# Optimization experiments

Hardware: AMD Instinct MI355X
Metric: run time of the kernel (lower is better)

Reference implementation:

```python
import jax, jax.numpy as jnp
import numpy as np

S_DIM = 8      # state_dim
O_DIM = 4      # obs_dim
HID = (S_DIM * S_DIM + O_DIM * O_DIM) * 10   # 800
BATCH = 128
SEQ = 32
NS = 16        # num_samples
P_DROP = 0.2
DROP_KEY = jax.random.key(42)

def f_dyn(x):
    # synthetic nonlinear dynamics (stand-in for system_model.f, vmapped over batch)
    return 0.9 * x + 0.1 * jnp.sin(x)

def h_obs(x):
    # synthetic nonlinear observation (stand-in for system_model.h)
    return jnp.tanh(x[..., :O_DIM])

def l2_normalize(x, eps=1e-12):
    # matches torch F.normalize(p=2, dim=1): x / max(||x||, eps)
    n = jnp.linalg.norm(x, axis=-1, keepdims=True)
    return x / jnp.maximum(n, eps)

def setup_inputs() -> dict:
    key = jax.random.key(0)
    ks = jax.random.split(key, 8)
    g = 0.02
    return {
        "y_seq": jax.random.normal(ks[0], (BATCH, SEQ, O_DIM), dtype=jnp.float32),
        "W1": jax.random.normal(ks[1], (HID, S_DIM + O_DIM), dtype=jnp.float32) * g,
        "b1": jnp.zeros((HID,), jnp.float32),
        "W_ih": jax.random.normal(ks[2], (3 * HID, HID), dtype=jnp.float32) * g,
        "W_hh": jax.random.normal(ks[3], (3 * HID, HID), dtype=jnp.float32) * g,
        "b_ih": jnp.zeros((3 * HID,), jnp.float32),
        "b_hh": jnp.zeros((3 * HID,), jnp.float32),
        "W_out": jax.random.normal(ks[4], (S_DIM * O_DIM, HID), dtype=jnp.float32) * g,
        "b_out": jnp.zeros((S_DIM * O_DIM,), jnp.float32),
        "num_samples": NS,
    }

def _forward(y_seq, W1, b1, W_ih, W_hh, b_ih, b_hh, W_out, b_out, num_samples):
    B = y_seq.shape[0]
    keep = 1.0 - P_DROP

    def gru_cell(x, h):
        # torch nn.GRU single-step math; x,h: [..., HID]
        gi = x @ W_ih.T + b_ih
        gh = h @ W_hh.T + b_hh
        gi_r, gi_z, gi_n = jnp.split(gi, 3, axis=-1)
        gh_r, gh_z, gh_n = jnp.split(gh, 3, axis=-1)
        r = jax.nn.sigmoid(gi_r + gh_r)
        z = jax.nn.sigmoid(gi_z + gh_z)
        n = jnp.tanh(gi_n + r * gh_n)
        return (1.0 - z) * n + z * h

    def step(carry, inp):
        x_prev, dx_prev, h_ens = carry            # [B,S], [B,S], [NS,B,HID]
        y_t, t = inp
        x_pred = f_dyn(x_prev)                    # [B,S] (same for every sample j)
        y_hat = h_obs(x_pred)                     # [B,O]
        innov = y_t - y_hat                       # [B,O]
        nn_in = jnp.concatenate([l2_normalize(dx_prev), l2_normalize(innov)], axis=-1)
        a = jax.nn.relu(nn_in @ W1.T + b1)        # [B,HID]
        k1, k2 = jax.random.split(jax.random.fold_in(DROP_KEY, t))
        m1 = jax.random.bernoulli(k1, keep, (num_samples, B, HID)).astype(a.dtype)
        a_ens = a[None] * m1 / keep               # MC-dropout per ensemble member
        h_new = gru_cell(a_ens, h_ens)            # [NS,B,HID] (vectorized over samples)
        K_vec = h_new @ W_out.T + b_out           # [NS,B,S*O]
        m2 = jax.random.bernoulli(k2, keep, K_vec.shape).astype(a.dtype)
        K = (K_vec * m2 / keep).reshape(num_samples, B, S_DIM, O_DIM)
        ens = x_pred[None] + jnp.einsum('jbso,bo->jbs', K, innov)  # [NS,B,S]
        x_filt = ens.mean(axis=0)                 # [B,S]
        diff = ens - x_filt[None]                 # [NS,B,S]
        P_filt = jnp.einsum('jbs,jbt->bst', diff, diff) / num_samples
        dx = x_filt - x_pred                      # delta_x_prev = x_filt - f(x_prev)
        return (x_filt, dx, h_new), (x_filt, P_filt)

    x0 = jnp.zeros((B, S_DIM), y_seq.dtype)
    dx0 = jnp.zeros((B, S_DIM), y_seq.dtype)
    h0 = jnp.zeros((num_samples, B, HID), y_seq.dtype)
    ts = jnp.arange(y_seq.shape[1])
    _, (xs, Ps) = jax.lax.scan(step, (x0, dx0, h0), (jnp.swapaxes(y_seq, 0, 1), ts))
    # xs: [T,B,S] -> [B,T,S]; Ps: [T,B,S,S] -> [B,T,S,S]
    return jnp.swapaxes(xs, 0, 1), jnp.swapaxes(Ps, 0, 1)

def reference(y_seq, W1, b1, W_ih, W_hh, b_ih, b_hh, W_out, b_out, num_samples):
    return _forward(y_seq, W1, b1, W_ih, W_hh, b_ih, b_hh, W_out, b_out, num_samples)
```

## Files before the change

kernel.cpp:

```cpp
#include <hip/hip_runtime.h>
#include <stdint.h>

#define NSAMP 16
#define BATCH 128
#define SEQLEN 32
#define SDIM 8
#define ODIM 4
#define HID 800
#define MROWS (NSAMP * BATCH)
#define KEEPP 0.8f

typedef __attribute__((ext_vector_type(8))) short short8v;
typedef __attribute__((ext_vector_type(4))) float float4v;

__host__ __device__ __forceinline__ void tf2x32(uint32_t k0, uint32_t k1,
                                                uint32_t x0, uint32_t x1,
                                                uint32_t& o0, uint32_t& o1) {
  uint32_t ks2 = k0 ^ k1 ^ 0x1BD11BDAu;
  x0 += k0; x1 += k1;
#define TFR(r) { x0 += x1; x1 = (x1 << (r)) | (x1 >> (32 - (r))); x1 ^= x0; }
  TFR(13) TFR(15) TFR(26) TFR(6)
  x0 += k1; x1 += ks2 + 1u;
  TFR(17) TFR(29) TFR(16) TFR(24)
  x0 += ks2; x1 += k0 + 2u;
  TFR(13) TFR(15) TFR(26) TFR(6)
  x0 += k0; x1 += k1 + 3u;
  TFR(17) TFR(29) TFR(16) TFR(24)
  x0 += k1; x1 += ks2 + 4u;
  TFR(13) TFR(15) TFR(26) TFR(6)
  x0 += ks2; x1 += k0 + 5u;
#undef TFR
  o0 = x0; o1 = x1;
}

__device__ __forceinline__ float bits_to_unit(uint32_t bits) {
  return __uint_as_float((bits >> 9) | 0x3F800000u) - 1.0f;
}

__device__ __forceinline__ float tf_uniform_part(uint32_t k0, uint32_t k1, uint32_t idx) {
  uint32_t b1, b2;
  tf2x32(k0, k1, 0u, idx, b1, b2);
  return bits_to_unit(b1 ^ b2);
}

__device__ __forceinline__ ushort f2bf(float f) {
  uint32_t u = __float_as_uint(f);
  uint32_t r = (u + 0x7FFFu + ((u >> 16) & 1u)) >> 16;
  return (ushort)r;
}

__device__ __forceinline__ float bf2f(ushort u) {
  return __uint_as_float((uint32_t)u << 16);
}

__device__ __forceinline__ void bar_sync() {
  __builtin_amdgcn_sched_barrier(0);
  __builtin_amdgcn_s_barrier();
  __builtin_amdgcn_sched_barrier(0);
}

__global__ void convert_w_kernel(const float* __restrict__ W_ih, const float* __restrict__ W_hh,
                                 ushort* __restrict__ Wib, ushort* __restrict__ Whb) {
  int i = (blockIdx.x * 256 + threadIdx.x) * 4;
  if (i >= 2400 * HID) return;
  float4 v1 = *reinterpret_cast<const float4*>(W_ih + i);
  float4 v2 = *reinterpret_cast<const float4*>(W_hh + i);
  ushort4 o1, o2;
  o1.x = f2bf(v1.x); o1.y = f2bf(v1.y); o1.z = f2bf(v1.z); o1.w = f2bf(v1.w);
  o2.x = f2bf(v2.x); o2.y = f2bf(v2.y); o2.z = f2bf(v2.z); o2.w = f2bf(v2.w);
  *reinterpret_cast<ushort4*>(Wib + i) = o1;
  *reinterpret_cast<ushort4*>(Whb + i) = o2;
}

__global__ void transpose_wout_kernel(const float* __restrict__ W_out, float* __restrict__ WoutT) {
  int i = blockIdx.x * 256 + threadIdx.x;
  if (i < 32 * HID) {
    int o = i / HID, k = i - o * HID;
    WoutT[k * 32 + o] = W_out[i];
  }
}

__global__ void a_ens_kernel(const float* __restrict__ a, ushort* __restrict__ aeb,
                             uint32_t k0, uint32_t k1) {
  int base = (blockIdx.x * blockDim.x + threadIdx.x) * 4;
  if (base >= MROWS * HID) return;
  int row = base / HID;
  int b = row % BATCH;
  int col = base - row * HID;
  float4 av = *reinterpret_cast<const float4*>(a + b * HID + col);
  ushort4 ov;
#pragma unroll
  for (int q = 0; q < 4; ++q) {
    float u = tf_uniform_part(k0, k1, (uint32_t)(base + q));
    float f = (&av.x)[q] * ((u < KEEPP) ? 1.25f : 0.0f);
    (&ov.x)[q] = f2bf(f);
  }
  *reinterpret_cast<ushort4*>(aeb + base) = ov;
}

#define LDSB 12288

__global__ __launch_bounds__(256, 2) void gru_mfma_kernel(
    const ushort* __restrict__ aeb, const ushort* __restrict__ hb,
    const ushort* __restrict__ Wib, const ushort* __restrict__ Whb,
    const float* __restrict__ h_old,
    const float* __restrict__ b_ih, const float* __restrict__ b_hh,
    float* __restrict__ h_new, ushort* __restrict__ h_new_b) {
  __shared__ __align__(1024) char lds[4 * LDSB];

  const int tid = threadIdx.x;
  const int wid = tid >> 6;
  const int lane = tid & 63;

  const int bid = blockIdx.x;
  const int xcd = bid & 7;
  const int q = bid >> 3;
  const int mm = q / 25;
  const int nblk = q - mm * 25;
  const int m0 = (xcd * 2 + mm) * 128;
  const int n0 = nblk * 32;

  float4v acc[6][2][2];
#pragma unroll
  for (int g = 0; g < 6; ++g)
#pragma unroll
    for (int mf = 0; mf < 2; ++mf)
#pragma unroll
      for (int nf = 0; nf < 2; ++nf)
        acc[g][mf][nf] = (float4v)(0.0f);

  const int rlo = lane >> 2;
  const int sslot = (lane & 3) ^ ((lane >> 3) & 3);
  const int kg = lane >> 4;
  const int l15 = lane & 15;

  const ushort* gp[3];
  int ldso[3];
#pragma unroll
  for (int s = 0; s < 3; ++s) {
    int i = s * 4 + wid;
    int g = i >> 1, half = i & 1;
    ldso[s] = g * 2048 + half * 1024;
    const ushort* base = (g < 3) ? Wib : Whb;
    int wrow = n0 + (g % 3) * HID + half * 16 + rlo;
    gp[s] = base + (size_t)wrow * HID + sslot * 8;
  }

  const ushort* ap[2][2];
#pragma unroll
  for (int mf = 0; mf < 2; ++mf) {
    const int row = m0 + wid * 32 + mf * 16 + l15;
    ap[0][mf] = aeb + (size_t)row * HID + kg * 8;
    ap[1][mf] = hb + (size_t)row * HID + kg * 8;
  }

  short8v ar0[2][2], ar1[2][2];

#define STAGE_T(BUFI) do {                                                       \
    _Pragma("unroll")                                                            \
    for (int s = 0; s < 3; ++s) {                                                \
      __builtin_amdgcn_global_load_lds(                                          \
          (const __attribute__((address_space(1))) void*)gp[s],                  \
          (__attribute__((address_space(3))) void*)(lds + (BUFI)*LDSB + ldso[s]),\
          16, 0, 0);                                                             \
      gp[s] += 32;                                                               \
    }                                                                            \
  } while (0)

#define LOAD_A(SET) do {                                                         \
    _Pragma("unroll")                                                            \
    for (int s2 = 0; s2 < 2; ++s2)                                               \
      _Pragma("unroll")                                                          \
      for (int mf = 0; mf < 2; ++mf) {                                           \
        SET[s2][mf] = *reinterpret_cast<const short8v*>(ap[s2][mf]);             \
        ap[s2][mf] += 32;                                                        \
      }                                                                          \
  } while (0)

#define COMPUTE(BUFI, SET) do {                                                  \
    const char* lb = lds + (BUFI)*LDSB;                                          \
    short8v bfr[6][2];                                                           \
    _Pragma("unroll")                                                            \
    for (int g = 0; g < 6; ++g)                                                  \
      _Pragma("unroll")                                                          \
      for (int nf = 0; nf < 2; ++nf) {                                           \
        int row = nf * 16 + l15;                                                 \
        int off = g * 2048 + row * 64 + ((kg ^ ((row >> 1) & 3)) << 4);          \
        bfr[g][nf] = *reinterpret_cast<const short8v*>(lb + off);                \
      }                                                                          \
    __builtin_amdgcn_s_setprio(1);                                               \
    _Pragma("unroll")                                                            \
    for (int g = 0; g < 6; ++g) {                                                \
      const int src = (g < 3) ? 0 : 1;                                           \
      _Pragma("unroll")                                                          \
      for (int mf = 0; mf < 2; ++mf)                                             \
        _Pragma("unroll")                                                        \
        for (int nf = 0; nf < 2; ++nf)                                           \
          acc[g][mf][nf] = __builtin_amdgcn_mfma_f32_16x16x32_bf16(              \
              SET[src][mf], bfr[g][nf], acc[g][mf][nf], 0, 0, 0);                \
    }                                                                            \
    __builtin_amdgcn_s_setprio(0);                                               \
  } while (0)

  STAGE_T(0);
  LOAD_A(ar0);
  STAGE_T(1);

#pragma unroll 1
  for (int p = 0; p < 22; p += 2) {
    LOAD_A(ar1);
    STAGE_T((p + 2) & 3);
    asm volatile("s_waitcnt vmcnt(10)" ::: "memory");
    bar_sync();
    COMPUTE(p & 3, ar0);
    LOAD_A(ar0);
    STAGE_T((p + 3) & 3);
    asm volatile("s_waitcnt vmcnt(10)" ::: "memory");
    bar_sync();
    COMPUTE((p + 1) & 3, ar1);
  }
  LOAD_A(ar1);
  STAGE_T(0);
  asm volatile("s_waitcnt vmcnt(10)" ::: "memory");
  bar_sync();
  COMPUTE(2, ar0);
  LOAD_A(ar0);
  asm volatile("s_waitcnt vmcnt(7)" ::: "memory");
  bar_sync();
  COMPUTE(3, ar1);
  asm volatile("s_waitcnt vmcnt(0)" ::: "memory");
  bar_sync();
  COMPUTE(0, ar0);

  const int rowq = (lane >> 4) * 4;
#pragma unroll
  for (int nf = 0; nf < 2; ++nf) {
    const int col = n0 + nf * 16 + l15;
    const float bir = b_ih[col], biz = b_ih[col + HID], bin = b_ih[col + 2 * HID];
    const float bhr = b_hh[col], bhz = b_hh[col + HID], bhn = b_hh[col + 2 * HID];
#pragma unroll
    for (int mf = 0; mf < 2; ++mf) {
#pragma unroll
      for (int reg = 0; reg < 4; ++reg) {
        const int m = m0 + wid * 32 + mf * 16 + rowq + reg;
        float gir = acc[0][mf][nf][reg] + bir;
        float giz = acc[1][mf][nf][reg] + biz;
        float gin = acc[2][mf][nf][reg] + bin;
        float ghr = acc[3][mf][nf][reg] + bhr;
        float ghz = acc[4][mf][nf][reg] + bhz;
        float ghn = acc[5][mf][nf][reg] + bhn;
        float r = 1.0f / (1.0f + expf(-(gir + ghr)));
        float z = 1.0f / (1.0f + expf(-(giz + ghz)));
        float nval = tanhf(gin + r * ghn);
        float hv = h_old[(size_t)m * HID + col];
        float res = (1.0f - z) * nval + z * hv;
        h_new[(size_t)m * HID + col] = res;
        h_new_b[(size_t)m * HID + col] = f2bf(res);
      }
    }
  }
#undef STAGE_T
#undef LOAD_A
#undef COMPUTE
}

__global__ void kvec_ens_kernel(const ushort* __restrict__ hnb,
                                const float* __restrict__ WoutT,
                                const float* __restrict__ b_out,
                                const float* __restrict__ x_pred,
                                const float* __restrict__ innov,
                                float* __restrict__ ens,
                                uint32_t k0, uint32_t k1) {
  const int jb = blockIdx.x;
  const int b = jb & (BATCH - 1);
  const int tid = threadIdx.x;
  const int o = tid & 31;
  const int kk = tid >> 5;

  const ushort* hrow = hnb + (size_t)jb * HID + kk * 100;
  const float* wc = WoutT + kk * 100 * 32 + o;
  float partial = 0.0f;
  for (int k = 0; k < 100; ++k)
    partial = fmaf(bf2f(hrow[k]), wc[k * 32], partial);

  __shared__ float red[8][32];
  __shared__ float Kv[32];
  red[kk][o] = partial;
  __syncthreads();
  if (tid < 32) {
    float s = 0.0f;
#pragma unroll
    for (int q = 0; q < 8; ++q) s += red[q][tid];
    s += b_out[tid];
    float u = tf_uniform_part(k0, k1, (uint32_t)(jb * 32 + tid));
    Kv[tid] = (u < KEEPP) ? s * 1.25f : 0.0f;
  }
  __syncthreads();
  if (tid < SDIM) {
    float s = x_pred[b * SDIM + tid];
#pragma unroll
    for (int oo = 0; oo < ODIM; ++oo)
      s = fmaf(Kv[tid * ODIM + oo], innov[b * ODIM + oo], s);
    ens[jb * SDIM + tid] = s;
  }
}

__global__ void reduce_prep_kernel(const float* __restrict__ ens,
                                   float* __restrict__ x_pred,
                                   float* __restrict__ innov,
                                   const float* __restrict__ y_seq,
                                   const float* __restrict__ W1,
                                   const float* __restrict__ b1,
                                   float* __restrict__ a,
                                   float* __restrict__ out_xs, float* __restrict__ out_Ps,
                                   int t) {
  const int b = blockIdx.x;
  const int tid = threadIdx.x;
  __shared__ float e[NSAMP][SDIM];
  __shared__ float xf[SDIM];
  __shared__ float dxs[SDIM];
  __shared__ float xpn[SDIM];
  __shared__ float inv[ODIM];
  __shared__ float nin[SDIM + ODIM];

  if (t >= 0) {
    if (tid < NSAMP * SDIM) {
      int j = tid >> 3, s = tid & 7;
      e[j][s] = ens[(j * BATCH + b) * SDIM + s];
    }
    __syncthreads();
    if (tid < SDIM) {
      float s = 0.0f;
#pragma unroll
      for (int j = 0; j < NSAMP; ++j) s += e[j][tid];
      s *= (1.0f / NSAMP);
      xf[tid] = s;
      out_xs[(b * SEQLEN + t) * SDIM + tid] = s;
      dxs[tid] = s - x_pred[b * SDIM + tid];
    }
    __syncthreads();
    if (tid < SDIM * SDIM) {
      int s = tid >> 3, u = tid & 7;
      float accv = 0.0f;
#pragma unroll
      for (int j = 0; j < NSAMP; ++j)
        accv += (e[j][s] - xf[s]) * (e[j][u] - xf[u]);
      out_Ps[((b * SEQLEN + t) * SDIM + s) * SDIM + u] = accv * (1.0f / NSAMP);
    }
  } else {
    if (tid < SDIM) { xf[tid] = 0.0f; dxs[tid] = 0.0f; }
  }
  if (t == SEQLEN - 1) return;
  __syncthreads();
  if (tid < SDIM) {
    float x = xf[tid];
    float xp = 0.9f * x + 0.1f * sinf(x);
    xpn[tid] = xp;
    x_pred[b * SDIM + tid] = xp;
  }
  __syncthreads();
  if (tid < ODIM) {
    float yh = tanhf(xpn[tid]);
    float iv = y_seq[(b * SEQLEN + (t + 1)) * ODIM + tid] - yh;
    inv[tid] = iv;
    innov[b * ODIM + tid] = iv;
  }
  __syncthreads();
  if (tid == 0) {
    float nd = 0.0f;
    for (int s = 0; s < SDIM; ++s) nd += dxs[s] * dxs[s];
    nd = fmaxf(sqrtf(nd), 1e-12f);
    for (int s = 0; s < SDIM; ++s) nin[s] = dxs[s] / nd;
    float ni = 0.0f;
    for (int o2 = 0; o2 < ODIM; ++o2) ni += inv[o2] * inv[o2];
    ni = fmaxf(sqrtf(ni), 1e-12f);
    for (int o2 = 0; o2 < ODIM; ++o2) nin[SDIM + o2] = inv[o2] / ni;
  }
  __syncthreads();
  for (int i = tid; i < HID; i += blockDim.x) {
    float s = b1[i];
#pragma unroll
    for (int c = 0; c < 12; ++c) s = fmaf(nin[c], W1[i * 12 + c], s);
    a[b * HID + i] = fmaxf(s, 0.0f);
  }
}

extern "C" void kernel_launch(void* const* d_in, const int* in_sizes, int n_in,
                              void* d_out, int out_size, void* d_ws, size_t ws_size,
                              hipStream_t stream) {
  (void)in_sizes; (void)n_in; (void)out_size; (void)ws_size;
  const float* y_seq = (const float*)d_in[0];
  const float* W1 = (const float*)d_in[1];
  const float* b1 = (const float*)d_in[2];
  const float* W_ih = (const float*)d_in[3];
  const float* W_hh = (const float*)d_in[4];
  const float* b_ih = (const float*)d_in[5];
  const float* b_hh = (const float*)d_in[6];
  const float* W_out = (const float*)d_in[7];
  const float* b_out = (const float*)d_in[8];

  char* ws = (char*)d_ws;
  size_t off = 0;
  float* h_a = (float*)(ws + off);    off += (size_t)MROWS * HID * 4;
  float* h_b = (float*)(ws + off);    off += (size_t)MROWS * HID * 4;
  ushort* hb_a = (ushort*)(ws + off); off += (size_t)MROWS * HID * 2;
  ushort* hb_b = (ushort*)(ws + off); off += (size_t)MROWS * HID * 2;
  ushort* aeb = (ushort*)(ws + off);  off += (size_t)MROWS * HID * 2;
  ushort* Wib = (ushort*)(ws + off);  off += (size_t)2400 * HID * 2;
  ushort* Whb = (ushort*)(ws + off);  off += (size_t)2400 * HID * 2;
  float* a_buf = (float*)(ws + off);  off += (size_t)BATCH * HID * 4;
  float* WoutT = (float*)(ws + off);  off += (size_t)HID * 32 * 4;
  float* x_pred = (float*)(ws + off); off += (size_t)BATCH * SDIM * 4;
  float* innov = (float*)(ws + off);  off += (size_t)BATCH * ODIM * 4;
  float* ens = (float*)(ws + off);    off += (size_t)NSAMP * BATCH * SDIM * 4;

  float* out_xs = (float*)d_out;
  float* out_Ps = out_xs + (size_t)BATCH * SEQLEN * SDIM;

  hipMemsetAsync(h_a, 0, (size_t)MROWS * HID * 4, stream);
  hipMemsetAsync(hb_a, 0, (size_t)MROWS * HID * 2, stream);
  convert_w_kernel<<<1875, 256, 0, stream>>>(W_ih, W_hh, Wib, Whb);
  transpose_wout_kernel<<<100, 256, 0, stream>>>(W_out, WoutT);
  reduce_prep_kernel<<<BATCH, 256, 0, stream>>>(ens, x_pred, innov, y_seq, W1, b1,
                                                a_buf, out_xs, out_Ps, -1);

  float* hc = h_a;  float* hn = h_b;
  ushort* hcb = hb_a; ushort* hnb = hb_b;
  for (int t = 0; t < SEQLEN; ++t) {
    uint32_t kt0, kt1, k1a, k1b, k2a, k2b;
    tf2x32(0u, 42u, 0u, (uint32_t)t, kt0, kt1);
    tf2x32(kt0, kt1, 0u, 0u, k1a, k1b);
    tf2x32(kt0, kt1, 0u, 1u, k2a, k2b);

    a_ens_kernel<<<1600, 256, 0, stream>>>(a_buf, aeb, k1a, k1b);
    gru_mfma_kernel<<<400, 256, 0, stream>>>(aeb, hcb, Wib, Whb, hc, b_ih, b_hh, hn, hnb);
    kvec_ens_kernel<<<MROWS, 256, 0, stream>>>(hnb, WoutT, b_out, x_pred, innov, ens, k2a, k2b);
    reduce_prep_kernel<<<BATCH, 256, 0, stream>>>(ens, x_pred, innov, y_seq, W1, b1,
                                                  a_buf, out_xs, out_Ps, t);
    float* tmp = hc; hc = hn; hn = tmp;
    ushort* tmpb = hcb; hcb = hnb; hnb = tmpb;
  }
}
```

Measured before the change: 1.828 ms.

## Keep full per-block GRU weight slice resident in LDS with prepacked layout

Weights are pre-packed once into per-16-column blocks with a padded row stride. Each GRU block loads its whole K-range weight slice (about 152 KB) into dynamic LDS up front, then streams activations from global with no per-tile barriers. The launch changes to 200 blocks of 512 threads, each covering 512 rows by 16 columns. This removes the multi-buffer staging and barrier synchronisation. In exchange, activation traffic doubles because of the narrower N tile, and the large LDS footprint limits each CU to one block while leaving some CUs idle.

New measurement: 2.043 ms. 1.12x slower.

```diff
diff --git a/kernel.cpp b/kernel.cpp
--- a/kernel.cpp
+++ b/kernel.cpp
@@ -9,6 +9,11 @@
 #define HID 800
 #define MROWS (NSAMP * BATCH)
 #define KEEPP 0.8f
+
+#define WPK_NBLK 77824
+#define WPK_G 12928
+#define WPK_C 808
+#define GRU_LDS_BYTES 155648
 
 typedef __attribute__((ext_vector_type(8))) short short8v;
 typedef __attribute__((ext_vector_type(4))) float float4v;
@@ -53,23 +58,18 @@
   return __uint_as_float((uint32_t)u << 16);
 }
 
-__device__ __forceinline__ void bar_sync() {
-  __builtin_amdgcn_sched_barrier(0);
-  __builtin_amdgcn_s_barrier();
-  __builtin_amdgcn_sched_barrier(0);
-}
-
-__global__ void convert_w_kernel(const float* __restrict__ W_ih, const float* __restrict__ W_hh,
-                                 ushort* __restrict__ Wib, ushort* __restrict__ Whb) {
-  int i = (blockIdx.x * 256 + threadIdx.x) * 4;
-  if (i >= 2400 * HID) return;
-  float4 v1 = *reinterpret_cast<const float4*>(W_ih + i);
-  float4 v2 = *reinterpret_cast<const float4*>(W_hh + i);
-  ushort4 o1, o2;
-  o1.x = f2bf(v1.x); o1.y = f2bf(v1.y); o1.z = f2bf(v1.z); o1.w = f2bf(v1.w);
-  o2.x = f2bf(v2.x); o2.y = f2bf(v2.y); o2.z = f2bf(v2.z); o2.w = f2bf(v2.w);
-  *reinterpret_cast<ushort4*>(Wib + i) = o1;
-  *reinterpret_cast<ushort4*>(Whb + i) = o2;
+__global__ void pack_w_kernel(const float* __restrict__ W_ih, const float* __restrict__ W_hh,
+                              ushort* __restrict__ Wpk) {
+  const int blk = blockIdx.x;
+  const int nblk = blk / 6, g = blk % 6;
+  const float* W = (g < 3) ? W_ih : W_hh;
+  const int grow = (g % 3) * HID;
+  ushort* dst = Wpk + (size_t)nblk * WPK_NBLK + (size_t)g * WPK_G;
+  for (int idx = threadIdx.x; idx < 16 * WPK_C; idx += 256) {
+    int c = idx / WPK_C, k = idx - c * WPK_C;
+    float v = (k < HID) ? W[(size_t)(grow + nblk * 16 + c) * HID + k] : 0.0f;
+    dst[c * WPK_C + k] = f2bf(v);
+  }
 }
 
 __global__ void transpose_wout_kernel(const float* __restrict__ W_out, float* __restrict__ WoutT) {
@@ -98,170 +98,120 @@
   *reinterpret_cast<ushort4*>(aeb + base) = ov;
 }
 
-#define LDSB 12288
-
-__global__ __launch_bounds__(256, 2) void gru_mfma_kernel(
+__global__ __launch_bounds__(512, 2) void gru_mfma_kernel(
     const ushort* __restrict__ aeb, const ushort* __restrict__ hb,
-    const ushort* __restrict__ Wib, const ushort* __restrict__ Whb,
+    const ushort* __restrict__ Wpk,
     const float* __restrict__ h_old,
     const float* __restrict__ b_ih, const float* __restrict__ b_hh,
     float* __restrict__ h_new, ushort* __restrict__ h_new_b) {
-  __shared__ __align__(1024) char lds[4 * LDSB];
+  extern __shared__ __align__(16) char lds[];
 
   const int tid = threadIdx.x;
-  const int wid = tid >> 6;
+  const int w = tid >> 6;
   const int lane = tid & 63;
+  const int l15 = lane & 15;
+  const int kg = lane >> 4;
 
   const int bid = blockIdx.x;
-  const int xcd = bid & 7;
-  const int q = bid >> 3;
-  const int mm = q / 25;
-  const int nblk = q - mm * 25;
-  const int m0 = (xcd * 2 + mm) * 128;
-  const int n0 = nblk * 32;
-
-  float4v acc[6][2][2];
+  const int nhalf = bid >> 3;
+  const int r3 = bid & 7;
+  const int mblk = r3 >> 1;
+  const int nblk = nhalf * 2 + (r3 & 1);
+  const int m0 = mblk * 512;
+  const int n0 = nblk * 16;
+
+  {
+    const ushort* wsrc = Wpk + (size_t)nblk * WPK_NBLK + (size_t)lane * 8;
+    for (int s = w * 19; s < w * 19 + 19; ++s) {
+      __builtin_amdgcn_global_load_lds(
+          (const __attribute__((address_space(1))) void*)(wsrc + (size_t)s * 512),
+          (__attribute__((address_space(3))) void*)(lds + s * 1024), 16, 0, 0);
+    }
+  }
+
+  float4v acc[6][4];
 #pragma unroll
   for (int g = 0; g < 6; ++g)
 #pragma unroll
-    for (int mf = 0; mf < 2; ++mf)
-#pragma unroll
-      for (int nf = 0; nf < 2; ++nf)
-        acc[g][mf][nf] = (float4v)(0.0f);
-
-  const int rlo = lane >> 2;
-  const int sslot = (lane & 3) ^ ((lane >> 3) & 3);
-  const int kg = lane >> 4;
-  const int l15 = lane & 15;
-
-  const ushort* gp[3];
-  int ldso[3];
-#pragma unroll
-  for (int s = 0; s < 3; ++s) {
-    int i = s * 4 + wid;
-    int g = i >> 1, half = i & 1;
-    ldso[s] = g * 2048 + half * 1024;
-    const ushort* base = (g < 3) ? Wib : Whb;
-    int wrow = n0 + (g % 3) * HID + half * 16 + rlo;
-    gp[s] = base + (size_t)wrow * HID + sslot * 8;
-  }
-
-  const ushort* ap[2][2];
-#pragma unroll
-  for (int mf = 0; mf < 2; ++mf) {
-    const int row = m0 + wid * 32 + mf * 16 + l15;
+    for (int mf = 0; mf < 4; ++mf)
+      acc[g][mf] = (float4v)(0.0f);
+
+  const ushort* ap[2][4];
+#pragma unroll
+  for (int mf = 0; mf < 4; ++mf) {
+    const int row = m0 + w * 64 + mf * 16 + l15;
     ap[0][mf] = aeb + (size_t)row * HID + kg * 8;
     ap[1][mf] = hb + (size_t)row * HID + kg * 8;
   }
-
-  short8v ar0[2][2], ar1[2][2];
-
-#define STAGE_T(BUFI) do {                                                       \
-    _Pragma("unroll")                                                            \
-    for (int s = 0; s < 3; ++s) {                                                \
-      __builtin_amdgcn_global_load_lds(                                          \
-          (const __attribute__((address_space(1))) void*)gp[s],                  \
-          (__attribute__((address_space(3))) void*)(lds + (BUFI)*LDSB + ldso[s]),\
-          16, 0, 0);                                                             \
-      gp[s] += 32;                                                               \
-    }                                                                            \
-  } while (0)
-
-#define LOAD_A(SET) do {                                                         \
+  short8v ar0[2][4], ar1[2][4];
+
+#define LOADA(SET) do {                                                          \
     _Pragma("unroll")                                                            \
     for (int s2 = 0; s2 < 2; ++s2)                                               \
       _Pragma("unroll")                                                          \
-      for (int mf = 0; mf < 2; ++mf) {                                           \
+      for (int mf = 0; mf < 4; ++mf) {                                           \
         SET[s2][mf] = *reinterpret_cast<const short8v*>(ap[s2][mf]);             \
         ap[s2][mf] += 32;                                                        \
       }                                                                          \
   } while (0)
 
-#define COMPUTE(BUFI, SET) do {                                                  \
-    const char* lb = lds + (BUFI)*LDSB;                                          \
-    short8v bfr[6][2];                                                           \
+#define COMP(T, SET) do {                                                        \
+    short8v bfr[6];                                                              \
     _Pragma("unroll")                                                            \
     for (int g = 0; g < 6; ++g)                                                  \
-      _Pragma("unroll")                                                          \
-      for (int nf = 0; nf < 2; ++nf) {                                           \
-        int row = nf * 16 + l15;                                                 \
-        int off = g * 2048 + row * 64 + ((kg ^ ((row >> 1) & 3)) << 4);          \
-        bfr[g][nf] = *reinterpret_cast<const short8v*>(lb + off);                \
-      }                                                                          \
+      bfr[g] = *reinterpret_cast<const short8v*>(                                \
+          lds + g * 25856 + l15 * 1616 + (T) * 64 + kg * 16);                    \
     __builtin_amdgcn_s_setprio(1);                                               \
     _Pragma("unroll")                                                            \
     for (int g = 0; g < 6; ++g) {                                                \
       const int src = (g < 3) ? 0 : 1;                                           \
       _Pragma("unroll")                                                          \
-      for (int mf = 0; mf < 2; ++mf)                                             \
-        _Pragma("unroll")                                                        \
-        for (int nf = 0; nf < 2; ++nf)                                           \
-          acc[g][mf][nf] = __builtin_amdgcn_mfma_f32_16x16x32_bf16(              \
-              SET[src][mf], bfr[g][nf], acc[g][mf][nf], 0, 0, 0);                \
+      for (int mf = 0; mf < 4; ++mf)                                             \
+        acc[g][mf] = __builtin_amdgcn_mfma_f32_16x16x32_bf16(                    \
+            SET[src][mf], bfr[g], acc[g][mf], 0, 0, 0);                          \
     }                                                                            \
     __builtin_amdgcn_s_setprio(0);                                               \
   } while (0)
 
-  STAGE_T(0);
-  LOAD_A(ar0);
-  STAGE_T(1);
+  LOADA(ar0);
+  asm volatile("s_waitcnt vmcnt(0)" ::: "memory");
+  __syncthreads();
 
 #pragma unroll 1
-  for (int p = 0; p < 22; p += 2) {
-    LOAD_A(ar1);
-    STAGE_T((p + 2) & 3);
-    asm volatile("s_waitcnt vmcnt(10)" ::: "memory");
-    bar_sync();
-    COMPUTE(p & 3, ar0);
-    LOAD_A(ar0);
-    STAGE_T((p + 3) & 3);
-    asm volatile("s_waitcnt vmcnt(10)" ::: "memory");
-    bar_sync();
-    COMPUTE((p + 1) & 3, ar1);
-  }
-  LOAD_A(ar1);
-  STAGE_T(0);
-  asm volatile("s_waitcnt vmcnt(10)" ::: "memory");
-  bar_sync();
-  COMPUTE(2, ar0);
-  LOAD_A(ar0);
-  asm volatile("s_waitcnt vmcnt(7)" ::: "memory");
-  bar_sync();
-  COMPUTE(3, ar1);
-  asm volatile("s_waitcnt vmcnt(0)" ::: "memory");
-  bar_sync();
-  COMPUTE(0, ar0);
+  for (int t = 0; t < 24; t += 2) {
+    LOADA(ar1);
+    COMP(t, ar0);
+    LOADA(ar0);
+    COMP(t + 1, ar1);
+  }
+  COMP(24, ar0);
 
   const int rowq = (lane >> 4) * 4;
-#pragma unroll
-  for (int nf = 0; nf < 2; ++nf) {
-    const int col = n0 + nf * 16 + l15;
-    const float bir = b_ih[col], biz = b_ih[col + HID], bin = b_ih[col + 2 * HID];
-    const float bhr = b_hh[col], bhz = b_hh[col + HID], bhn = b_hh[col + 2 * HID];
-#pragma unroll
-    for (int mf = 0; mf < 2; ++mf) {
-#pragma unroll
-      for (int reg = 0; reg < 4; ++reg) {
-        const int m = m0 + wid * 32 + mf * 16 + rowq + reg;
-        float gir = acc[0][mf][nf][reg] + bir;
-        float giz = acc[1][mf][nf][reg] + biz;
-        float gin = acc[2][mf][nf][reg] + bin;
-        float ghr = acc[3][mf][nf][reg] + bhr;
-        float ghz = acc[4][mf][nf][reg] + bhz;
-        float ghn = acc[5][mf][nf][reg] + bhn;
-        float r = 1.0f / (1.0f + expf(-(gir + ghr)));
-        float z = 1.0f / (1.0f + expf(-(giz + ghz)));
-        float nval = tanhf(gin + r * ghn);
-        float hv = h_old[(size_t)m * HID + col];
-        float res = (1.0f - z) * nval + z * hv;
-        h_new[(size_t)m * HID + col] = res;
-        h_new_b[(size_t)m * HID + col] = f2bf(res);
-      }
-    }
-  }
-#undef STAGE_T
-#undef LOAD_A
-#undef COMPUTE
+  const int col = n0 + l15;
+  const float bir = b_ih[col], biz = b_ih[col + HID], bin = b_ih[col + 2 * HID];
+  const float bhr = b_hh[col], bhz = b_hh[col + HID], bhn = b_hh[col + 2 * HID];
+#pragma unroll
+  for (int mf = 0; mf < 4; ++mf) {
+#pragma unroll
+    for (int reg = 0; reg < 4; ++reg) {
+      const int m = m0 + w * 64 + mf * 16 + rowq + reg;
+      float gir = acc[0][mf][reg] + bir;
+      float giz = acc[1][mf][reg] + biz;
+      float gin = acc[2][mf][reg] + bin;
+      float ghr = acc[3][mf][reg] + bhr;
+      float ghz = acc[4][mf][reg] + bhz;
+      float ghn = acc[5][mf][reg] + bhn;
+      float r = 1.0f / (1.0f + expf(-(gir + ghr)));
+      float z = 1.0f / (1.0f + expf(-(giz + ghz)));
+      float nval = tanhf(gin + r * ghn);
+      float hv = h_old[(size_t)m * HID + col];
+      float res = (1.0f - z) * nval + z * hv;
+      h_new[(size_t)m * HID + col] = res;
+      h_new_b[(size_t)m * HID + col] = f2bf(res);
+    }
+  }
+#undef LOADA
+#undef COMP
 }
 
 __global__ void kvec_ens_kernel(const ushort* __restrict__ hnb,
@@ -406,8 +356,7 @@
   ushort* hb_a = (ushort*)(ws + off); off += (size_t)MROWS * HID * 2;
   ushort* hb_b = (ushort*)(ws + off); off += (size_t)MROWS * HID * 2;
   ushort* aeb = (ushort*)(ws + off);  off += (size_t)MROWS * HID * 2;
-  ushort* Wib = (ushort*)(ws + off);  off += (size_t)2400 * HID * 2;
-  ushort* Whb = (ushort*)(ws + off);  off += (size_t)2400 * HID * 2;
+  ushort* Wpk = (ushort*)(ws + off);  off += (size_t)50 * WPK_NBLK * 2;
   float* a_buf = (float*)(ws + off);  off += (size_t)BATCH * HID * 4;
   float* WoutT = (float*)(ws + off);  off += (size_t)HID * 32 * 4;
   float* x_pred = (float*)(ws + off); off += (size_t)BATCH * SDIM * 4;
@@ -417,9 +366,12 @@
   float* out_xs = (float*)d_out;
   float* out_Ps = out_xs + (size_t)BATCH * SEQLEN * SDIM;
 
+  (void)hipFuncSetAttribute(reinterpret_cast<const void*>(&gru_mfma_kernel),
+                            hipFuncAttributeMaxDynamicSharedMemorySize, GRU_LDS_BYTES);
+
   hipMemsetAsync(h_a, 0, (size_t)MROWS * HID * 4, stream);
   hipMemsetAsync(hb_a, 0, (size_t)MROWS * HID * 2, stream);
-  convert_w_kernel<<<1875, 256, 0, stream>>>(W_ih, W_hh, Wib, Whb);
+  pack_w_kernel<<<300, 256, 0, stream>>>(W_ih, W_hh, Wpk);
   transpose_wout_kernel<<<100, 256, 0, stream>>>(W_out, WoutT);
   reduce_prep_kernel<<<BATCH, 256, 0, stream>>>(ens, x_pred, innov, y_seq, W1, b1,
                                                 a_buf, out_xs, out_Ps, -1);
@@ -433,7 +385,8 @@
     tf2x32(kt0, kt1, 0u, 1u, k2a, k2b);
 
     a_ens_kernel<<<1600, 256, 0, stream>>>(a_buf, aeb, k1a, k1b);
-    gru_mfma_kernel<<<400, 256, 0, stream>>>(aeb, hcb, Wib, Whb, hc, b_ih, b_hh, hn, hnb);
+    gru_mfma_kernel<<<200, 512, GRU_LDS_BYTES, stream>>>(aeb, hcb, Wpk, hc,
+                                                         b_ih, b_hh, hn, hnb);
     kvec_ens_kernel<<<MROWS, 256, 0, stream>>>(hnb, WoutT, b_out, x_pred, innov, ens, k2a, k2b);
     reduce_prep_kernel<<<BATCH, 256, 0, stream>>>(ens, x_pred, innov, y_seq, W1, b1,
                                                   a_buf, out_xs, out_Ps, t);
```
